# Optimization experiments

Hardware: AMD Instinct MI355X
Metric: run time of the kernel (lower is better)

## Reference

```python
import jax, jax.numpy as jnp
import numpy as np

B, T, N_EMBS, HEAD = 8, 2048, 1024, 64


def setup_inputs() -> dict:
    key = jax.random.key(0)
    k1, k2, k3, k4 = jax.random.split(key, 4)
    x = jax.random.normal(k1, (B, T, N_EMBS), dtype=jnp.float32)
    # nn.Linear(n_embs, head_size, bias=False): y = x @ W^T with W [head, n_embs].
    # We store the transposed weight [n_embs, head] directly for clean einsum.
    s = 1.0 / np.sqrt(N_EMBS)
    Wk = jax.random.uniform(k2, (N_EMBS, HEAD), jnp.float32, -s, s)
    Wq = jax.random.uniform(k3, (N_EMBS, HEAD), jnp.float32, -s, s)
    Wv = jax.random.uniform(k4, (N_EMBS, HEAD), jnp.float32, -s, s)
    return {"x": x, "Wk": Wk, "Wq": Wq, "Wv": Wv}


def reference(x, Wk, Wq, Wv):
    # Single causal self-attention head (dropout rate = 0.0).
    k = jnp.einsum("btn,nh->bth", x, Wk)  # [B,T,H]
    q = jnp.einsum("btn,nh->bth", x, Wq)
    v = jnp.einsum("btn,nh->bth", x, Wv)
    scale = k.shape[-1] ** -0.5
    scores = jnp.einsum("bqh,bkh->bqk", q, k) * scale  # [B,T,T]
    t = x.shape[1]
    causal = jnp.tril(jnp.ones((t, t), dtype=bool))
    scores = jnp.where(causal, scores, -jnp.inf)
    attn = jax.nn.softmax(scores, axis=-1)
    return jnp.einsum("bqk,bkh->bqh", attn, v)  # [B,T,H]
```

## Files before the change

kernel.cpp:

```cpp
#include <hip/hip_runtime.h>
#include <math.h>

#define BB 8
#define TT 2048
#define NE 1024
#define HH 64
#define BT (BB * TT)

typedef __attribute__((ext_vector_type(8))) short s8v;
typedef __attribute__((ext_vector_type(4))) float f4v;

__device__ inline unsigned short f2bf(float f) {
  union { float f; unsigned u; } v;
  v.f = f;
  unsigned r = (v.u + 0x7FFFu + ((v.u >> 16) & 1u)) >> 16;
  return (unsigned short)r;
}

__device__ inline unsigned short f2bf_trunc(float f) {
  union { float f; unsigned u; } v;
  v.f = f;
  return (unsigned short)(v.u >> 16);
}

__device__ inline unsigned cvtpk(float lo, float hi) {
  unsigned r;
  asm("v_cvt_pk_bf16_f32 %0, %1, %2" : "=v"(r) : "v"(lo), "v"(hi));
  return r;
}

__device__ inline void glds16(const unsigned short* g, unsigned short* l) {
  __builtin_amdgcn_global_load_lds(
      (const __attribute__((address_space(1))) unsigned*)g,
      (__attribute__((address_space(3))) unsigned*)l, 16, 0, 0);
}

__global__ __launch_bounds__(256) void conv_wt_kernel(
    const float* __restrict__ Wq, const float* __restrict__ Wk,
    const float* __restrict__ Wv, unsigned short* __restrict__ WTswz) {
  const int idx = blockIdx.x * 256 + threadIdx.x;
  const int r = idx >> 7;
  const int c8 = idx & 127;
  const int l8 = (c8 & ~7) | ((c8 & 7) ^ (r & 7));
  const int n0 = l8 * 8;
  const int m = r >> 6, h = r & 63;
  const float* W = (m == 0) ? Wq : (m == 1) ? Wk : Wv;
  unsigned short v[8];
#pragma unroll
  for (int j = 0; j < 8; ++j) v[j] = f2bf(W[(size_t)(n0 + j) * HH + h]);
  *reinterpret_cast<uint4*>(WTswz + (size_t)r * NE + c8 * 8) =
      *reinterpret_cast<const uint4*>(v);
}

__global__ __launch_bounds__(256, 2) void qkv_proj_mfma(
    const float* __restrict__ x, const unsigned short* __restrict__ WTswz,
    unsigned short* __restrict__ Q, unsigned short* __restrict__ K,
    unsigned short* __restrict__ VT) {
  __shared__ __align__(16) unsigned short Abuf[2][32 * 72];
  __shared__ __align__(16) unsigned short Bbuf[2][192 * 64];

  const int tid = threadIdx.x;
  const int lane = tid & 63;
  const int w = tid >> 6;
  const int rg = w & 1, cg = w >> 1;
  const int lr = lane & 15, lg = lane >> 4;
  const int row0 = blockIdx.x * 32;

  const int arow = tid >> 3, aunit = tid & 7;
  const float* __restrict__ xrow = x + (size_t)(row0 + arow) * NE + aunit * 8;
  unsigned short* const awr = &Abuf[0][0] + arow * 72 + aunit * 8;

  const int bcol = w * 48 + (lane >> 3);
  const unsigned short* const bsrc0 =
      WTswz + (size_t)bcol * NE + (lane & 7) * 8;
  unsigned short* const bdst0 = &Bbuf[0][0] + (w * 48) * 64;

  f4v acc[6];
#pragma unroll
  for (int c = 0; c < 6; ++c) acc[c] = (f4v)0.f;

  float4 a0 = *reinterpret_cast<const float4*>(xrow);
  float4 a1 = *reinterpret_cast<const float4*>(xrow + 4);
#pragma unroll
  for (int j = 0; j < 6; ++j)
    glds16(bsrc0 + (size_t)j * 8 * NE, bdst0 + j * 512);
  {
    unsigned au[4] = {cvtpk(a0.x, a0.y), cvtpk(a0.z, a0.w),
                      cvtpk(a1.x, a1.y), cvtpk(a1.z, a1.w)};
    *reinterpret_cast<uint4*>(awr) = *reinterpret_cast<const uint4*>(au);
  }
  __syncthreads();

  int cur = 0;
  for (int t = 0; t < 16; ++t) {
    const int kcn = (t + 1) * 64;
    if (t < 15) {
      a0 = *reinterpret_cast<const float4*>(xrow + kcn);
      a1 = *reinterpret_cast<const float4*>(xrow + kcn + 4);
#pragma unroll
      for (int j = 0; j < 6; ++j)
        glds16(bsrc0 + (size_t)j * 8 * NE + kcn,
               bdst0 + (cur ^ 1) * 12288 + j * 512);
    }
    const unsigned short* Ab = &Abuf[cur][0];
    const unsigned short* Bb = &Bbuf[cur][0];
#pragma unroll
    for (int ks = 0; ks < 2; ++ks) {
      const s8v a = *reinterpret_cast<const s8v*>(
          Ab + (rg * 16 + lr) * 72 + ks * 32 + lg * 8);
#pragma unroll
      for (int c = 0; c < 6; ++c) {
        const int col = cg * 96 + c * 16 + lr;
        const int uraw = (lg + ks * 4) ^ (lr & 7);
        const s8v b = *reinterpret_cast<const s8v*>(Bb + col * 64 + uraw * 8);
        acc[c] = __builtin_amdgcn_mfma_f32_16x16x32_bf16(a, b, acc[c], 0, 0, 0);
      }
    }
    if (t < 15) {
      unsigned au[4] = {cvtpk(a0.x, a0.y), cvtpk(a0.z, a0.w),
                        cvtpk(a1.x, a1.y), cvtpk(a1.z, a1.w)};
      *reinterpret_cast<uint4*>(awr + (cur ^ 1) * 2304) =
          *reinterpret_cast<const uint4*>(au);
      __syncthreads();
      cur ^= 1;
    }
  }

#pragma unroll
  for (int c = 0; c < 6; ++c) {
    const int col = cg * 96 + c * 16 + lr;
    const int m = col >> 6;
    const int h = col & 63;
#pragma unroll
    for (int r = 0; r < 4; ++r) {
      const int rr = row0 + rg * 16 + lg * 4 + r;
      const unsigned short bv = f2bf(acc[c][r]);
      if (m == 0) {
        Q[(size_t)rr * HH + h] = bv;
      } else if (m == 1) {
        K[(size_t)rr * HH + h] = bv;
      } else {
        const int bb = rr >> 11, tt2 = rr & (TT - 1);
        VT[((size_t)bb * HH + h) * TT + tt2] = bv;
      }
    }
  }
}

__global__ __launch_bounds__(256, 4) void flash_attn_mfma(
    const unsigned short* __restrict__ Q, const unsigned short* __restrict__ K,
    const unsigned short* __restrict__ VT, float* __restrict__ out) {
  __shared__ unsigned short pl[4][16][72];
  __shared__ float ol[4][16][64];
  __shared__ float ml[4][16];
  __shared__ float ll[4][16];

  const int tid = threadIdx.x;
  const int lane = tid & 63;
  const int w = tid >> 6;
  const int lr = lane & 15;
  const int lg = lane >> 4;
  const int bid = blockIdx.x;
  const int b = bid & 7;
  const int qt = bid >> 3;
  const int q0 = qt * 16;
  const size_t rowbase = (size_t)b * TT;
  const float SCL = 0.18033688011112042f;

  const int nt = (qt >> 2) + 1;
  const int base = nt >> 2, rem = nt & 3;
  const int t0 = w * base + (w < rem ? w : rem);
  const int cnt = base + (w < rem ? 1 : 0);

  const s8v qf0 = *reinterpret_cast<const s8v*>(
      Q + (rowbase + q0 + lr) * HH + lg * 8);
  const s8v qf1 = *reinterpret_cast<const s8v*>(
      Q + (rowbase + q0 + lr) * HH + 32 + lg * 8);

  f4v o[4];
#pragma unroll
  for (int n = 0; n < 4; ++n) o[n] = (f4v)0.f;
  float mrow[4], lrow[4];
#pragma unroll
  for (int r = 0; r < 4; ++r) { mrow[r] = -INFINITY; lrow[r] = 0.f; }

  for (int kt = t0; kt < t0 + cnt; ++kt) {
    const int k0 = kt * 64;
    f4v s[4];
#pragma unroll
    for (int nk = 0; nk < 4; ++nk) s[nk] = (f4v)0.f;
#pragma unroll
    for (int nk = 0; nk < 4; ++nk) {
      const unsigned short* kp = K + (rowbase + k0 + 16 * nk + lr) * HH + lg * 8;
      const s8v kf0 = *reinterpret_cast<const s8v*>(kp);
      const s8v kf1 = *reinterpret_cast<const s8v*>(kp + 32);
      s[nk] = __builtin_amdgcn_mfma_f32_16x16x32_bf16(qf0, kf0, s[nk], 0, 0, 0);
      s[nk] = __builtin_amdgcn_mfma_f32_16x16x32_bf16(qf1, kf1, s[nk], 0, 0, 0);
    }
    s8v vfr[2][4];
#pragma unroll
    for (int kh = 0; kh < 2; ++kh)
#pragma unroll
      for (int n = 0; n < 4; ++n)
        vfr[kh][n] = *reinterpret_cast<const s8v*>(
            VT + ((size_t)b * HH + 16 * n + lr) * TT + k0 + kh * 32 + lg * 8);

    const bool diag = (kt == nt - 1);
#pragma unroll
    for (int nk = 0; nk < 4; ++nk) {
#pragma unroll
      for (int r = 0; r < 4; ++r) {
        float v = s[nk][r] * SCL;
        if (diag) {
          const int kk = k0 + 16 * nk + lr;
          const int qq = q0 + lg * 4 + r;
          if (kk > qq) v = -INFINITY;
        }
        s[nk][r] = v;
      }
    }
    float scl[4];
#pragma unroll
    for (int r = 0; r < 4; ++r) {
      float mx = fmaxf(fmaxf(s[0][r], s[1][r]), fmaxf(s[2][r], s[3][r]));
#pragma unroll
      for (int off = 1; off < 16; off <<= 1)
        mx = fmaxf(mx, __shfl_xor(mx, off));
      const float mnew = fmaxf(mrow[r], mx);
      scl[r] = exp2f(mrow[r] - mnew);
      mrow[r] = mnew;
      float rs = 0.f;
#pragma unroll
      for (int nk = 0; nk < 4; ++nk) {
        const float p = exp2f(s[nk][r] - mnew);
        s[nk][r] = p;
        rs += p;
      }
#pragma unroll
      for (int off = 1; off < 16; off <<= 1)
        rs += __shfl_xor(rs, off);
      lrow[r] = lrow[r] * scl[r] + rs;
    }
#pragma unroll
    for (int n = 0; n < 4; ++n)
#pragma unroll
      for (int r = 0; r < 4; ++r) o[n][r] *= scl[r];
#pragma unroll
    for (int nk = 0; nk < 4; ++nk)
#pragma unroll
      for (int r = 0; r < 4; ++r)
        pl[w][lg * 4 + r][16 * nk + lr] = f2bf_trunc(s[nk][r]);
#pragma unroll
    for (int kh = 0; kh < 2; ++kh) {
      const int pc = kh * 32 + lg * 8;
      const ushort4 plo = *reinterpret_cast<const ushort4*>(&pl[w][lr][pc]);
      const ushort4 phi = *reinterpret_cast<const ushort4*>(&pl[w][lr][pc + 4]);
      s8v pa;
      pa[0] = plo.x; pa[1] = plo.y; pa[2] = plo.z; pa[3] = plo.w;
      pa[4] = phi.x; pa[5] = phi.y; pa[6] = phi.z; pa[7] = phi.w;
#pragma unroll
      for (int n = 0; n < 4; ++n)
        o[n] = __builtin_amdgcn_mfma_f32_16x16x32_bf16(pa, vfr[kh][n], o[n], 0, 0, 0);
    }
  }

#pragma unroll
  for (int n = 0; n < 4; ++n)
#pragma unroll
    for (int r = 0; r < 4; ++r) ol[w][lg * 4 + r][16 * n + lr] = o[n][r];
  if (lr == 0) {
#pragma unroll
    for (int r = 0; r < 4; ++r) {
      ml[w][lg * 4 + r] = mrow[r];
      ll[w][lg * 4 + r] = lrow[r];
    }
  }
  __syncthreads();

  const int row = tid >> 4;
  const int c0 = (tid & 15) * 4;
  float m0 = ml[0][row], m1 = ml[1][row], m2 = ml[2][row], m3 = ml[3][row];
  const float ms = fmaxf(fmaxf(m0, m1), fmaxf(m2, m3));
  const float w0 = exp2f(m0 - ms), w1 = exp2f(m1 - ms);
  const float w2 = exp2f(m2 - ms), w3 = exp2f(m3 - ms);
  const float lsum = w0 * ll[0][row] + w1 * ll[1][row] +
                     w2 * ll[2][row] + w3 * ll[3][row];
  float4 osum;
  osum.x = w0 * ol[0][row][c0 + 0] + w1 * ol[1][row][c0 + 0] +
           w2 * ol[2][row][c0 + 0] + w3 * ol[3][row][c0 + 0];
  osum.y = w0 * ol[0][row][c0 + 1] + w1 * ol[1][row][c0 + 1] +
           w2 * ol[2][row][c0 + 1] + w3 * ol[3][row][c0 + 1];
  osum.z = w0 * ol[0][row][c0 + 2] + w1 * ol[1][row][c0 + 2] +
           w2 * ol[2][row][c0 + 2] + w3 * ol[3][row][c0 + 2];
  osum.w = w0 * ol[0][row][c0 + 3] + w1 * ol[1][row][c0 + 3] +
           w2 * ol[2][row][c0 + 3] + w3 * ol[3][row][c0 + 3];
  const float inv = 1.0f / lsum;
  float4 res;
  res.x = osum.x * inv; res.y = osum.y * inv;
  res.z = osum.z * inv; res.w = osum.w * inv;
  *reinterpret_cast<float4*>(out + (rowbase + q0 + row) * HH + c0) = res;
}

extern "C" void kernel_launch(void* const* d_in, const int* in_sizes, int n_in,
                              void* d_out, int out_size, void* d_ws, size_t ws_size,
                              hipStream_t stream) {
  const float* x  = (const float*)d_in[0];
  const float* Wk = (const float*)d_in[1];
  const float* Wq = (const float*)d_in[2];
  const float* Wv = (const float*)d_in[3];
  float* out = (float*)d_out;

  unsigned short* ws = (unsigned short*)d_ws;
  unsigned short* Q  = ws;
  unsigned short* K  = ws + (size_t)BT * HH;
  unsigned short* VT = ws + 2 * (size_t)BT * HH;
  unsigned short* WT = ws + 3 * (size_t)BT * HH;

  conv_wt_kernel<<<96, 256, 0, stream>>>(Wq, Wk, Wv, WT);
  qkv_proj_mfma<<<512, 256, 0, stream>>>(x, WT, Q, K, VT);
  flash_attn_mfma<<<1024, 256, 0, stream>>>(Q, K, VT, out);
}
```

Measured before the change: 77.37 us.

## Fold softmax scale into Q, lazy max rescale, reverse tile order, MFMA priority

Folds the softmax scale (including log2e) into Q at projection time, which removes a multiply per score in the attention loop. Adds FA4-style lazy rescaling: the running max and the O/l rescale are updated only when some row's max grows by more than 8 (in log2 units) anywhere in the wave. Reverses the query-tile order so the heaviest causal blocks launch first, and raises wave priority around MFMA sections with s_setprio. The risks are skipped rescales letting intermediate values grow by up to 2^8, and extra rounding from storing the scaled Q in bf16.

```diff
diff --git a/kernel.cpp b/kernel.cpp
--- a/kernel.cpp
+++ b/kernel.cpp
@@ -126,6 +126,7 @@
     }
   }
 
+  const float QSCL = 0.18033688011112042f;
 #pragma unroll
   for (int c = 0; c < 6; ++c) {
     const int col = cg * 96 + c * 16 + lr;
@@ -134,14 +135,13 @@
 #pragma unroll
     for (int r = 0; r < 4; ++r) {
       const int rr = row0 + rg * 16 + lg * 4 + r;
-      const unsigned short bv = f2bf(acc[c][r]);
       if (m == 0) {
-        Q[(size_t)rr * HH + h] = bv;
+        Q[(size_t)rr * HH + h] = f2bf(acc[c][r] * QSCL);
       } else if (m == 1) {
-        K[(size_t)rr * HH + h] = bv;
+        K[(size_t)rr * HH + h] = f2bf(acc[c][r]);
       } else {
         const int bb = rr >> 11, tt2 = rr & (TT - 1);
-        VT[((size_t)bb * HH + h) * TT + tt2] = bv;
+        VT[((size_t)bb * HH + h) * TT + tt2] = f2bf(acc[c][r]);
       }
     }
   }
@@ -162,10 +162,9 @@
   const int lg = lane >> 4;
   const int bid = blockIdx.x;
   const int b = bid & 7;
-  const int qt = bid >> 3;
+  const int qt = 127 - (bid >> 3);
   const int q0 = qt * 16;
   const size_t rowbase = (size_t)b * TT;
-  const float SCL = 0.18033688011112042f;
 
   const int nt = (qt >> 2) + 1;
   const int base = nt >> 2, rem = nt & 3;
@@ -189,6 +188,7 @@
     f4v s[4];
 #pragma unroll
     for (int nk = 0; nk < 4; ++nk) s[nk] = (f4v)0.f;
+    __builtin_amdgcn_s_setprio(1);
 #pragma unroll
     for (int nk = 0; nk < 4; ++nk) {
       const unsigned short* kp = K + (rowbase + k0 + 16 * nk + lr) * HH + lg * 8;
@@ -197,6 +197,7 @@
       s[nk] = __builtin_amdgcn_mfma_f32_16x16x32_bf16(qf0, kf0, s[nk], 0, 0, 0);
       s[nk] = __builtin_amdgcn_mfma_f32_16x16x32_bf16(qf1, kf1, s[nk], 0, 0, 0);
     }
+    __builtin_amdgcn_s_setprio(0);
     s8v vfr[2][4];
 #pragma unroll
     for (int kh = 0; kh < 2; ++kh)
@@ -205,46 +206,54 @@
         vfr[kh][n] = *reinterpret_cast<const s8v*>(
             VT + ((size_t)b * HH + 16 * n + lr) * TT + k0 + kh * 32 + lg * 8);
 
-    const bool diag = (kt == nt - 1);
-#pragma unroll
-    for (int nk = 0; nk < 4; ++nk) {
-#pragma unroll
-      for (int r = 0; r < 4; ++r) {
-        float v = s[nk][r] * SCL;
-        if (diag) {
-          const int kk = k0 + 16 * nk + lr;
+    if (kt == nt - 1) {
+#pragma unroll
+      for (int nk = 0; nk < 4; ++nk) {
+        const int kk = k0 + 16 * nk + lr;
+#pragma unroll
+        for (int r = 0; r < 4; ++r) {
           const int qq = q0 + lg * 4 + r;
-          if (kk > qq) v = -INFINITY;
+          if (kk > qq) s[nk][r] = -INFINITY;
         }
-        s[nk][r] = v;
-      }
-    }
-    float scl[4];
+      }
+    }
+
+    float mx_[4];
+    float grow = -INFINITY;
 #pragma unroll
     for (int r = 0; r < 4; ++r) {
       float mx = fmaxf(fmaxf(s[0][r], s[1][r]), fmaxf(s[2][r], s[3][r]));
 #pragma unroll
       for (int off = 1; off < 16; off <<= 1)
         mx = fmaxf(mx, __shfl_xor(mx, off));
-      const float mnew = fmaxf(mrow[r], mx);
-      scl[r] = exp2f(mrow[r] - mnew);
-      mrow[r] = mnew;
+      mx_[r] = mx;
+      grow = fmaxf(grow, mx - mrow[r]);
+    }
+    if (!__all(grow <= 8.f)) {
+#pragma unroll
+      for (int r = 0; r < 4; ++r) {
+        const float mnew = fmaxf(mrow[r], mx_[r]);
+        const float scl = exp2f(mrow[r] - mnew);
+        mrow[r] = mnew;
+        lrow[r] *= scl;
+#pragma unroll
+        for (int n = 0; n < 4; ++n) o[n][r] *= scl;
+      }
+    }
+#pragma unroll
+    for (int r = 0; r < 4; ++r) {
       float rs = 0.f;
 #pragma unroll
       for (int nk = 0; nk < 4; ++nk) {
-        const float p = exp2f(s[nk][r] - mnew);
+        const float p = exp2f(s[nk][r] - mrow[r]);
         s[nk][r] = p;
         rs += p;
       }
 #pragma unroll
       for (int off = 1; off < 16; off <<= 1)
         rs += __shfl_xor(rs, off);
-      lrow[r] = lrow[r] * scl[r] + rs;
-    }
-#pragma unroll
-    for (int n = 0; n < 4; ++n)
-#pragma unroll
-      for (int r = 0; r < 4; ++r) o[n][r] *= scl[r];
+      lrow[r] += rs;
+    }
 #pragma unroll
     for (int nk = 0; nk < 4; ++nk)
 #pragma unroll
@@ -258,9 +267,11 @@
       s8v pa;
       pa[0] = plo.x; pa[1] = plo.y; pa[2] = plo.z; pa[3] = plo.w;
       pa[4] = phi.x; pa[5] = phi.y; pa[6] = phi.z; pa[7] = phi.w;
+      __builtin_amdgcn_s_setprio(1);
 #pragma unroll
       for (int n = 0; n < 4; ++n)
         o[n] = __builtin_amdgcn_mfma_f32_16x16x32_bf16(pa, vfr[kh][n], o[n], 0, 0, 0);
+      __builtin_amdgcn_s_setprio(0);
     }
   }
 
```

After: 73.00 us. 5.7% less time.
